# Performance work log

Hardware: AMD Instinct MI355X
Metric: run time of the kernel (lower is better)

## Reference

```python
import jax, jax.numpy as jnp
import numpy as np

N, E, IN_FT, OUT_FT = 8192, 4096, 512, 512
DENSITY = 0.02


def setup_inputs() -> dict:
    key = jax.random.key(0)
    k1, k2, k3, k4 = jax.random.split(key, 4)
    x = jax.random.normal(k1, (N, IN_FT), dtype=jnp.float32)
    hypergraph = (jax.random.uniform(k2, (N, E)) < DENSITY).astype(jnp.float32)
    # kaiming_uniform on [in, out]: fan_in = in_ft (torch fan of a Linear-style 2D param is dim 1 size? torch computes fan_in = size(1) for 2D -> out_ft here)
    bound_w = float(np.sqrt(6.0 / OUT_FT))  # kaiming_uniform a=sqrt(5)? default a=0 -> gain sqrt(2); bound = gain*sqrt(3/fan_in)
    bound_w = float(np.sqrt(2.0) * np.sqrt(3.0 / OUT_FT))
    weight = jax.random.uniform(k3, (IN_FT, OUT_FT), minval=-bound_w, maxval=bound_w, dtype=jnp.float32)
    bound_v = float(np.sqrt(2.0) * np.sqrt(3.0 / 1.0))
    V = jax.random.uniform(k4, (IN_FT, 1), minval=-bound_v, maxval=bound_v, dtype=jnp.float32)
    bias = jnp.zeros((OUT_FT,), dtype=jnp.float32)
    return {"x": x, "hypergraph": hypergraph, "weight": weight, "V": V, "bias": bias}


def reference(x, hypergraph, weight, V, bias):
    # edge embeddings: H^T @ x  -> [E, in_ft]
    edge_emb = hypergraph.T @ x
    hw = jax.nn.sigmoid(edge_emb @ V)          # [E, 1] learned hyperedge weights
    w = hw[:, 0]                                # [E]
    deg_v = (hypergraph @ hw)[:, 0]             # [N]  (sum over last dim of H @ hw)
    deg_e = jnp.sum(hypergraph, axis=0)         # [E]
    # adj = diag(deg_v) @ H @ diag(w) @ diag(deg_e) @ H^T @ diag(deg_v)
    # fused as broadcasted row/col scalings around two GEMMs (same math, no NxN)
    out = x @ weight                            # [N, out_ft]
    t = hypergraph.T @ (deg_v[:, None] * out)   # [E, out_ft]
    t = (w * deg_e)[:, None] * t                # diagonal edge scalings
    out = deg_v[:, None] * (hypergraph @ t)     # [N, out_ft]
    out = out + bias
    return (out, w)
```

## Files before the change

kernel.cpp:

```cpp
#include <hip/hip_runtime.h>


#define N_NODES 8192
#define N_EDGES 4096
#define FT 512

typedef short bf16x8 __attribute__((ext_vector_type(8)));
typedef float f32x4 __attribute__((ext_vector_type(4)));
typedef unsigned short u16;
typedef unsigned int u32;
typedef unsigned char u8;

__device__ __forceinline__ u16 f2b(float f) {
    union { float f; u32 u; } v; v.f = f;
    u32 r = v.u + 0x7FFFu + ((v.u >> 16) & 1u);
    return (u16)(r >> 16);
}
__device__ __forceinline__ float b2f(u16 h) {
    union { u32 u; float f; } v; v.u = ((u32)h) << 16; return v.f;
}
__device__ __forceinline__ u32 pack2(u32 w) {
    union { float f; u32 u; } a, b;
    a.f = (float)(w & 0xFFu);
    b.f = (float)((w >> 8) & 0xFFu);
    return __builtin_amdgcn_perm(b.u, a.u, 0x07060302u);
}


__global__ __launch_bounds__(256) void zero_kernel(float* p, int n) {
    int i = blockIdx.x * 256 + threadIdx.x;
    if (i < n) p[i] = 0.f;
}

__global__ __launch_bounds__(256) void xv_kernel(const float* __restrict__ x,
                                                 const float* __restrict__ V,
                                                 float* __restrict__ xv) {
    int row = blockIdx.x * 4 + (threadIdx.x >> 6);
    int lane = threadIdx.x & 63;
    const float* xr = x + (size_t)row * FT + lane * 8;
    const float* vr = V + lane * 8;
    float4 a0 = *(const float4*)xr, a1 = *(const float4*)(xr + 4);
    float4 b0 = *(const float4*)vr, b1 = *(const float4*)(vr + 4);
    float acc = a0.x * b0.x + a0.y * b0.y + a0.z * b0.z + a0.w * b0.w +
                a1.x * b1.x + a1.y * b1.y + a1.z * b1.z + a1.w * b1.w;
#pragma unroll
    for (int off = 32; off; off >>= 1) acc += __shfl_down(acc, off);
    if (lane == 0) xv[row] = acc;
}

__global__ __launch_bounds__(256) void cvt_colsum_kernel(const float* __restrict__ H,
                                                         const float* __restrict__ xv,
                                                         u8* __restrict__ Hu8,
                                                         float* __restrict__ zsum,
                                                         float* __restrict__ desum) {
    int e0 = (blockIdx.x * 256 + threadIdx.x) * 4;
    int n0 = blockIdx.y * 32;
    float z0 = 0.f, z1 = 0.f, z2 = 0.f, z3 = 0.f;
    float d0 = 0.f, d1 = 0.f, d2 = 0.f, d3 = 0.f;
#pragma unroll 4
    for (int i = 0; i < 32; i++) {
        int n = n0 + i;
        float4 h = *(const float4*)(H + (size_t)n * N_EDGES + e0);
        float xvn = xv[n];
        z0 += h.x * xvn; z1 += h.y * xvn; z2 += h.z * xvn; z3 += h.w * xvn;
        d0 += h.x; d1 += h.y; d2 += h.z; d3 += h.w;
        u32 p = (u32)h.x | ((u32)h.y << 8) | ((u32)h.z << 16) | ((u32)h.w << 24);
        *(u32*)(Hu8 + (size_t)n * N_EDGES + e0) = p;
    }
    atomicAdd(zsum + e0 + 0, z0); atomicAdd(zsum + e0 + 1, z1);
    atomicAdd(zsum + e0 + 2, z2); atomicAdd(zsum + e0 + 3, z3);
    atomicAdd(desum + e0 + 0, d0); atomicAdd(desum + e0 + 1, d1);
    atomicAdd(desum + e0 + 2, d2); atomicAdd(desum + e0 + 3, d3);
}

__global__ __launch_bounds__(256) void sigmoid_kernel(const float* __restrict__ zsum,
                                                      const float* __restrict__ desum,
                                                      float* __restrict__ w_out,
                                                      float* __restrict__ wde) {
    int e = blockIdx.x * 256 + threadIdx.x;
    float z = zsum[e];
    float wv = 1.f / (1.f + expf(-z));
    w_out[e] = wv;
    wde[e] = wv * desum[e];
}

__global__ __launch_bounds__(256) void degv_kernel(const u8* __restrict__ Hu8,
                                                   const float* __restrict__ w,
                                                   float* __restrict__ degv) {
    int row = blockIdx.x * 4 + (threadIdx.x >> 6);
    int lane = threadIdx.x & 63;
    const u32* hr = (const u32*)(Hu8 + (size_t)row * N_EDGES);
    const float4* wr = (const float4*)w;
    float acc = 0.f;
#pragma unroll
    for (int i = 0; i < 16; i++) {
        int idx = i * 64 + lane;
        u32 h4 = hr[idx];
        float4 ww = wr[idx];
        if (h4 & 0x000000FFu) acc += ww.x;
        if (h4 & 0x0000FF00u) acc += ww.y;
        if (h4 & 0x00FF0000u) acc += ww.z;
        if (h4 & 0xFF000000u) acc += ww.w;
    }
#pragma unroll
    for (int off = 32; off; off >>= 1) acc += __shfl_down(acc, off);
    if (lane == 0) degv[row] = acc;
}

__global__ void wt_kernel(const float* __restrict__ src, u16* __restrict__ dst) {
    __shared__ float tile[32][33];
    int tx = threadIdx.x, ty = threadIdx.y;
    int c = blockIdx.x * 32 + tx;
    int r0 = blockIdx.y * 32;
#pragma unroll
    for (int i = 0; i < 4; i++)
        tile[ty + i * 8][tx] = src[(size_t)(r0 + ty + i * 8) * FT + c];
    __syncthreads();
#pragma unroll
    for (int i = 0; i < 4; i++)
        dst[(size_t)(blockIdx.x * 32 + ty + i * 8) * FT + r0 + tx] = f2b(tile[tx][ty + i * 8]);
}

__global__ __launch_bounds__(256) void transH_kernel(const u8* __restrict__ Hu8,
                                                     u8* __restrict__ HTu8) {
    __shared__ u32 tile[64][17];
    const int t = threadIdx.x;
    const int e0 = blockIdx.x * 64, n0 = blockIdx.y * 64;
    {
        int nl = t >> 2, seg = t & 3;
        uint4 v = *(const uint4*)(Hu8 + (size_t)(n0 + nl) * N_EDGES + e0 + seg * 16);
        tile[nl][seg * 4 + 0] = v.x; tile[nl][seg * 4 + 1] = v.y;
        tile[nl][seg * 4 + 2] = v.z; tile[nl][seg * 4 + 3] = v.w;
    }
    __syncthreads();
    int ew = t >> 4, ng = t & 15;
    u32 a0 = tile[ng * 4 + 0][ew], a1 = tile[ng * 4 + 1][ew];
    u32 a2 = tile[ng * 4 + 2][ew], a3 = tile[ng * 4 + 3][ew];
#pragma unroll
    for (int i = 0; i < 4; i++) {
        u32 o = ((a0 >> (8 * i)) & 0xFFu) | (((a1 >> (8 * i)) & 0xFFu) << 8) |
                (((a2 >> (8 * i)) & 0xFFu) << 16) | (((a3 >> (8 * i)) & 0xFFu) << 24);
        *(u32*)(HTu8 + (size_t)(e0 + ew * 4 + i) * N_NODES + n0 + ng * 4) = o;
    }
}

__global__ void t2t_kernel(const u16* __restrict__ P, const float* __restrict__ wde,
                           u16* __restrict__ t2T) {
    __shared__ float tile[32][33];
    int tx = threadIdx.x, ty = threadIdx.y;
    int f0 = blockIdx.x * 32, e0 = blockIdx.y * 32;
#pragma unroll
    for (int i = 0; i < 4; i++) {
        int e = e0 + ty + i * 8;
        size_t idx = (size_t)e * 512 + f0 + tx;
        float s = 0.f;
#pragma unroll
        for (int sl = 0; sl < 8; sl++)
            s += b2f(P[idx + (size_t)sl * N_EDGES * 512]);
        tile[ty + i * 8][tx] = wde[e] * s;
    }
    __syncthreads();
#pragma unroll
    for (int i = 0; i < 4; i++)
        t2T[(size_t)(f0 + ty + i * 8) * N_EDGES + e0 + tx] = f2b(tile[tx][ty + i * 8]);
}

__global__ __launch_bounds__(256) void final_kernel(const u16* __restrict__ P,
                                                    const float* __restrict__ degv,
                                                    const float* __restrict__ bias,
                                                    float* __restrict__ out) {
    int i8 = blockIdx.x * 256 + threadIdx.x;
    int base = i8 * 8;
    int n = base >> 9, f = base & 511;
    float s[8] = {0.f, 0.f, 0.f, 0.f, 0.f, 0.f, 0.f, 0.f};
#pragma unroll
    for (int sl = 0; sl < 4; sl++) {
        uint4 v = *(const uint4*)(P + (size_t)sl * N_NODES * 512 + base);
        u32 ws[4] = {v.x, v.y, v.z, v.w};
#pragma unroll
        for (int j = 0; j < 4; j++) {
            s[2 * j]     += b2f((u16)(ws[j] & 0xFFFFu));
            s[2 * j + 1] += b2f((u16)(ws[j] >> 16));
        }
    }
    float dv = degv[n];
    float4 o0, o1;
    o0.x = dv * s[0] + bias[f + 0]; o0.y = dv * s[1] + bias[f + 1];
    o0.z = dv * s[2] + bias[f + 2]; o0.w = dv * s[3] + bias[f + 3];
    o1.x = dv * s[4] + bias[f + 4]; o1.y = dv * s[5] + bias[f + 5];
    o1.z = dv * s[6] + bias[f + 6]; o1.w = dv * s[7] + bias[f + 7];
    *(float4*)(out + base) = o0;
    *(float4*)(out + base + 4) = o1;
}


#define TBK 32

template <int MT, int NT, int ASRC, int BSRC, int EPI>
__global__ __launch_bounds__(256, 2)
void gemm5(const void* __restrict__ Ap, const void* __restrict__ Bp,
           void* __restrict__ Cp, const float* __restrict__ degv,
           int KC, int lda, int ldb, int ldc, int Msz) {
    __shared__ __align__(16) u16 Alds[MT * 32 * TBK];
    __shared__ __align__(16) u16 Blds[NT * 32 * TBK];
    const int t = threadIdx.x;
    const int m0 = blockIdx.x * (MT * 32), n0 = blockIdx.y * (NT * 32);
    const int kbase = blockIdx.z * KC;
    const int wave = t >> 6, lane = t & 63, quad = lane >> 4, lo = lane & 15;
    const int wm = (wave >> 1) * (MT * 16), wn = (wave & 1) * (NT * 16);

    f32x4 acc[MT][NT];
#pragma unroll
    for (int a = 0; a < MT; a++)
#pragma unroll
        for (int b = 0; b < NT; b++) acc[a][b] = (f32x4){0.f, 0.f, 0.f, 0.f};

    for (int kk = 0; kk < KC; kk += TBK) {
        const int k0 = kbase + kk;
        __syncthreads();
        if (ASRC == 0) {
            const u16* A = (const u16*)Ap;
#pragma unroll
            for (int i = 0; i < MT / 2; i++) {
                int c = t + i * 256;
                const u16* g = A + (size_t)(m0 + (c >> 2)) * lda + k0 + (c & 3) * 8;
                __builtin_amdgcn_global_load_lds((const u32*)g, (u32*)(Alds + c * 8), 16, 0, 0);
            }
        } else {
            const u8* A = (const u8*)Ap;
            const int r = t >> 1, h = (t & 1) * 16;
            uint4 v = *(const uint4*)(A + (size_t)(m0 + r) * lda + k0 + h);
            u32 o[8];
            o[0] = pack2(v.x); o[1] = pack2(v.x >> 16);
            o[2] = pack2(v.y); o[3] = pack2(v.y >> 16);
            o[4] = pack2(v.z); o[5] = pack2(v.z >> 16);
            o[6] = pack2(v.w); o[7] = pack2(v.w >> 16);
            *(uint4*)&Alds[r * TBK + h]     = *(uint4*)&o[0];
            *(uint4*)&Alds[r * TBK + h + 8] = *(uint4*)&o[4];
        }
        if (BSRC == 0) {
            const u16* B = (const u16*)Bp;
#pragma unroll
            for (int i = 0; i < NT / 2; i++) {
                int c = t + i * 256;
                const u16* g = B + (size_t)(n0 + (c >> 2)) * ldb + k0 + (c & 3) * 8;
                __builtin_amdgcn_global_load_lds((const u32*)g, (u32*)(Blds + c * 8), 16, 0, 0);
            }
        } else {
            const float* B = (const float*)Bp;
            const int n = t >> 1, c0 = (t & 1) * 16;
            const float4* src = (const float4*)(B + (size_t)(n0 + n) * ldb + k0 + c0);
            float4 f[4];
#pragma unroll
            for (int i = 0; i < 4; i++) f[i] = src[i];
            u16 tmp[16];
#pragma unroll
            for (int i = 0; i < 4; i++) {
                tmp[4 * i + 0] = f2b(f[i].x); tmp[4 * i + 1] = f2b(f[i].y);
                tmp[4 * i + 2] = f2b(f[i].z); tmp[4 * i + 3] = f2b(f[i].w);
            }
            *(uint4*)&Blds[n * TBK + c0]     = *(uint4*)&tmp[0];
            *(uint4*)&Blds[n * TBK + c0 + 8] = *(uint4*)&tmp[8];
        }
        __syncthreads();

        bf16x8 af[MT], bfr[NT];
#pragma unroll
        for (int mt = 0; mt < MT; mt++)
            af[mt] = *(const bf16x8*)&Alds[(wm + mt * 16 + lo) * TBK + quad * 8];
#pragma unroll
        for (int nt = 0; nt < NT; nt++)
            bfr[nt] = *(const bf16x8*)&Blds[(wn + nt * 16 + lo) * TBK + quad * 8];
#pragma unroll
        for (int mt = 0; mt < MT; mt++)
#pragma unroll
            for (int nt = 0; nt < NT; nt++)
                acc[mt][nt] = __builtin_amdgcn_mfma_f32_16x16x32_bf16(af[mt], bfr[nt], acc[mt][nt], 0, 0, 0);
    }

    if (EPI == 0) {
        u16* C = (u16*)Cp + (size_t)blockIdx.z * Msz * 512;
#pragma unroll
        for (int mt = 0; mt < MT; mt++) {
            int rb = m0 + wm + mt * 16 + quad * 4;
#pragma unroll
            for (int i = 0; i < 4; i++)
#pragma unroll
                for (int nt = 0; nt < NT; nt++)
                    C[(size_t)(rb + i) * 512 + n0 + wn + nt * 16 + lo] = f2b(acc[mt][nt][i]);
        }
    } else {
        u16* C = (u16*)Cp;
        float dv[NT];
#pragma unroll
        for (int nt = 0; nt < NT; nt++) dv[nt] = degv[n0 + wn + nt * 16 + lo];
#pragma unroll
        for (int mt = 0; mt < MT; mt++) {
            int rb = m0 + wm + mt * 16 + quad * 4;
#pragma unroll
            for (int i = 0; i < 4; i++)
#pragma unroll
                for (int nt = 0; nt < NT; nt++)
                    C[(size_t)(rb + i) * ldc + n0 + wn + nt * 16 + lo] =
                        f2b(acc[mt][nt][i] * dv[nt]);
        }
    }
}


extern "C" void kernel_launch(void* const* d_in, const int* in_sizes, int n_in,
                              void* d_out, int out_size, void* d_ws, size_t ws_size,
                              hipStream_t stream) {
    const float* x    = (const float*)d_in[0];
    const float* H    = (const float*)d_in[1];
    const float* W    = (const float*)d_in[2];
    const float* V    = (const float*)d_in[3];
    const float* bias = (const float*)d_in[4];
    float* out  = (float*)d_out;
    float* wout = out + (size_t)N_NODES * FT;
    (void)in_sizes; (void)n_in; (void)out_size; (void)ws_size;

    char* wsb = (char*)d_ws;
    float* wsf   = (float*)d_ws;
    float* xv    = wsf;
    float* zsum  = wsf + 8192;
    float* desum = wsf + 12288;
    float* wde   = wsf + 16384;
    float* degv  = wsf + 20480;
    u8*    Hu8   = (u8*)(wsb + 114688);
    u8*    HTu8  = (u8*)(wsb + 33669120);
    u16*   WT    = (u16*)(wsb + 67223552);
    u16*   doutT = (u16*)(wsb + 67747840);
    u16*   t2T   = (u16*)(wsb + 76136448);
    u16*   P     = (u16*)(wsb + 80330752);

    zero_kernel<<<32, 256, 0, stream>>>(zsum, 8192);
    xv_kernel<<<N_NODES / 4, 256, 0, stream>>>(x, V, xv);
    cvt_colsum_kernel<<<dim3(4, 256), 256, 0, stream>>>(H, xv, Hu8, zsum, desum);
    sigmoid_kernel<<<N_EDGES / 256, 256, 0, stream>>>(zsum, desum, wout, wde);
    degv_kernel<<<N_NODES / 4, 256, 0, stream>>>(Hu8, wout, degv);
    wt_kernel<<<dim3(16, 16), dim3(32, 8), 0, stream>>>(W, WT);
    transH_kernel<<<dim3(N_EDGES / 64, N_NODES / 64), 256, 0, stream>>>(Hu8, HTu8);

    gemm5<2, 4, 0, 2, 1><<<dim3(FT / 64, N_NODES / 128, 1), 256, 0, stream>>>(
        WT, x, doutT, degv, FT, FT, FT, N_NODES, 0);

    gemm5<4, 8, 1, 0, 0><<<dim3(N_EDGES / 128, FT / 256, 8), 256, 0, stream>>>(
        HTu8, doutT, P, nullptr, N_NODES / 8, N_NODES, N_NODES, 512, N_EDGES);

    t2t_kernel<<<dim3(FT / 32, N_EDGES / 32), dim3(32, 8), 0, stream>>>(P, wde, t2T);

    gemm5<4, 8, 1, 0, 0><<<dim3(N_NODES / 128, FT / 256, 4), 256, 0, stream>>>(
        Hu8, t2T, P, nullptr, N_EDGES / 4, N_EDGES, N_EDGES, 512, N_NODES);

    final_kernel<<<(N_NODES * FT / 8) / 256, 256, 0, stream>>>(P, degv, bias, out);
}
```

Baseline: 386.8 us.

## Store incidence and x as bf16 so GEMMs use direct global-to-LDS loads

The incidence matrix and its transpose are now stored as bf16 instead of u8, and x is pre-converted to bf16 inside the xv kernel. All GEMM operand loads can therefore use global_load_lds directly, with no in-register unpacking or fp32 conversion. The GEMM tiles also change from 4x8 to 4x4 with more N blocks, and the occupancy hint goes from 2 to 3. This doubles the memory traffic and footprint for H and H^T and adds an extra bf16 copy of x, in exchange for removing conversion work from the GEMM inner loops.

```diff
diff --git a/kernel.cpp b/kernel.cpp
--- a/kernel.cpp
+++ b/kernel.cpp
@@ -9,7 +9,6 @@
 typedef float f32x4 __attribute__((ext_vector_type(4)));
 typedef unsigned short u16;
 typedef unsigned int u32;
-typedef unsigned char u8;
 
 __device__ __forceinline__ u16 f2b(float f) {
     union { float f; u32 u; } v; v.f = f;
@@ -19,12 +18,6 @@
 __device__ __forceinline__ float b2f(u16 h) {
     union { u32 u; float f; } v; v.u = ((u32)h) << 16; return v.f;
 }
-__device__ __forceinline__ u32 pack2(u32 w) {
-    union { float f; u32 u; } a, b;
-    a.f = (float)(w & 0xFFu);
-    b.f = (float)((w >> 8) & 0xFFu);
-    return __builtin_amdgcn_perm(b.u, a.u, 0x07060302u);
-}
 
 
 __global__ __launch_bounds__(256) void zero_kernel(float* p, int n) {
@@ -32,9 +25,10 @@
     if (i < n) p[i] = 0.f;
 }
 
-__global__ __launch_bounds__(256) void xv_kernel(const float* __restrict__ x,
-                                                 const float* __restrict__ V,
-                                                 float* __restrict__ xv) {
+__global__ __launch_bounds__(256) void xv_xb_kernel(const float* __restrict__ x,
+                                                    const float* __restrict__ V,
+                                                    float* __restrict__ xv,
+                                                    u16* __restrict__ xb) {
     int row = blockIdx.x * 4 + (threadIdx.x >> 6);
     int lane = threadIdx.x & 63;
     const float* xr = x + (size_t)row * FT + lane * 8;
@@ -43,6 +37,9 @@
     float4 b0 = *(const float4*)vr, b1 = *(const float4*)(vr + 4);
     float acc = a0.x * b0.x + a0.y * b0.y + a0.z * b0.z + a0.w * b0.w +
                 a1.x * b1.x + a1.y * b1.y + a1.z * b1.z + a1.w * b1.w;
+    u16 tmp[8] = {f2b(a0.x), f2b(a0.y), f2b(a0.z), f2b(a0.w),
+                  f2b(a1.x), f2b(a1.y), f2b(a1.z), f2b(a1.w)};
+    *(uint4*)(xb + (size_t)row * FT + lane * 8) = *(uint4*)tmp;
 #pragma unroll
     for (int off = 32; off; off >>= 1) acc += __shfl_down(acc, off);
     if (lane == 0) xv[row] = acc;
@@ -50,7 +47,7 @@
 
 __global__ __launch_bounds__(256) void cvt_colsum_kernel(const float* __restrict__ H,
                                                          const float* __restrict__ xv,
-                                                         u8* __restrict__ Hu8,
+                                                         u16* __restrict__ Hbf,
                                                          float* __restrict__ zsum,
                                                          float* __restrict__ desum) {
     int e0 = (blockIdx.x * 256 + threadIdx.x) * 4;
@@ -64,8 +61,10 @@
         float xvn = xv[n];
         z0 += h.x * xvn; z1 += h.y * xvn; z2 += h.z * xvn; z3 += h.w * xvn;
         d0 += h.x; d1 += h.y; d2 += h.z; d3 += h.w;
-        u32 p = (u32)h.x | ((u32)h.y << 8) | ((u32)h.z << 16) | ((u32)h.w << 24);
-        *(u32*)(Hu8 + (size_t)n * N_EDGES + e0) = p;
+        uint2 p;
+        p.x = (h.x != 0.f ? 0x3F80u : 0u) | (h.y != 0.f ? 0x3F800000u : 0u);
+        p.y = (h.z != 0.f ? 0x3F80u : 0u) | (h.w != 0.f ? 0x3F800000u : 0u);
+        *(uint2*)(Hbf + (size_t)n * N_EDGES + e0) = p;
     }
     atomicAdd(zsum + e0 + 0, z0); atomicAdd(zsum + e0 + 1, z1);
     atomicAdd(zsum + e0 + 2, z2); atomicAdd(zsum + e0 + 3, z3);
@@ -84,23 +83,23 @@
     wde[e] = wv * desum[e];
 }
 
-__global__ __launch_bounds__(256) void degv_kernel(const u8* __restrict__ Hu8,
+__global__ __launch_bounds__(256) void degv_kernel(const u16* __restrict__ Hbf,
                                                    const float* __restrict__ w,
                                                    float* __restrict__ degv) {
     int row = blockIdx.x * 4 + (threadIdx.x >> 6);
     int lane = threadIdx.x & 63;
-    const u32* hr = (const u32*)(Hu8 + (size_t)row * N_EDGES);
-    const float4* wr = (const float4*)w;
+    const uint4* hr = (const uint4*)(Hbf + (size_t)row * N_EDGES);
     float acc = 0.f;
 #pragma unroll
-    for (int i = 0; i < 16; i++) {
+    for (int i = 0; i < 8; i++) {
         int idx = i * 64 + lane;
-        u32 h4 = hr[idx];
-        float4 ww = wr[idx];
-        if (h4 & 0x000000FFu) acc += ww.x;
-        if (h4 & 0x0000FF00u) acc += ww.y;
-        if (h4 & 0x00FF0000u) acc += ww.z;
-        if (h4 & 0xFF000000u) acc += ww.w;
+        uint4 h = hr[idx];
+        const float* w8 = w + idx * 8;
+        float4 wa = *(const float4*)w8, wb = *(const float4*)(w8 + 4);
+        if (h.x & 0xFFFFu) acc += wa.x;  if (h.x >> 16) acc += wa.y;
+        if (h.y & 0xFFFFu) acc += wa.z;  if (h.y >> 16) acc += wa.w;
+        if (h.z & 0xFFFFu) acc += wb.x;  if (h.z >> 16) acc += wb.y;
+        if (h.w & 0xFFFFu) acc += wb.z;  if (h.w >> 16) acc += wb.w;
     }
 #pragma unroll
     for (int off = 32; off; off >>= 1) acc += __shfl_down(acc, off);
@@ -121,26 +120,36 @@
         dst[(size_t)(blockIdx.x * 32 + ty + i * 8) * FT + r0 + tx] = f2b(tile[tx][ty + i * 8]);
 }
 
-__global__ __launch_bounds__(256) void transH_kernel(const u8* __restrict__ Hu8,
-                                                     u8* __restrict__ HTu8) {
-    __shared__ u32 tile[64][17];
+__global__ __launch_bounds__(256) void transHb_kernel(const u16* __restrict__ Hbf,
+                                                      u16* __restrict__ HTbf) {
+    __shared__ u32 Wt[64][33];
     const int t = threadIdx.x;
     const int e0 = blockIdx.x * 64, n0 = blockIdx.y * 64;
     {
-        int nl = t >> 2, seg = t & 3;
-        uint4 v = *(const uint4*)(Hu8 + (size_t)(n0 + nl) * N_EDGES + e0 + seg * 16);
-        tile[nl][seg * 4 + 0] = v.x; tile[nl][seg * 4 + 1] = v.y;
-        tile[nl][seg * 4 + 2] = v.z; tile[nl][seg * 4 + 3] = v.w;
+        int n = t >> 2, seg = t & 3;
+        const u16* src = Hbf + (size_t)(n0 + n) * N_EDGES + e0;
+#pragma unroll
+        for (int jj = 0; jj < 2; jj++) {
+            int j = seg + jj * 4;
+            uint4 v = *(const uint4*)(src + j * 8);
+            Wt[n][j * 4 + 0] = v.x; Wt[n][j * 4 + 1] = v.y;
+            Wt[n][j * 4 + 2] = v.z; Wt[n][j * 4 + 3] = v.w;
+        }
     }
     __syncthreads();
-    int ew = t >> 4, ng = t & 15;
-    u32 a0 = tile[ng * 4 + 0][ew], a1 = tile[ng * 4 + 1][ew];
-    u32 a2 = tile[ng * 4 + 2][ew], a3 = tile[ng * 4 + 3][ew];
-#pragma unroll
-    for (int i = 0; i < 4; i++) {
-        u32 o = ((a0 >> (8 * i)) & 0xFFu) | (((a1 >> (8 * i)) & 0xFFu) << 8) |
-                (((a2 >> (8 * i)) & 0xFFu) << 16) | (((a3 >> (8 * i)) & 0xFFu) << 24);
-        *(u32*)(HTu8 + (size_t)(e0 + ew * 4 + i) * N_NODES + n0 + ng * 4) = o;
+    {
+        int e = t >> 2, g = t & 3;
+        int ew = e >> 1;
+        u32 sel = (e & 1) ? 0x07060302u : 0x05040100u;
+        u32* drow = (u32*)(HTbf + (size_t)(e0 + e) * N_NODES + n0);
+        u32 o[8];
+#pragma unroll
+        for (int j = 0; j < 8; j++) {
+            int np = g * 8 + j;
+            o[j] = __builtin_amdgcn_perm(Wt[2 * np + 1][ew], Wt[2 * np][ew], sel);
+        }
+        *(uint4*)(drow + g * 8)     = *(uint4*)&o[0];
+        *(uint4*)(drow + g * 8 + 4) = *(uint4*)&o[4];
     }
 }
 
@@ -196,9 +205,9 @@
 
 #define TBK 32
 
-template <int MT, int NT, int ASRC, int BSRC, int EPI>
-__global__ __launch_bounds__(256, 2)
-void gemm5(const void* __restrict__ Ap, const void* __restrict__ Bp,
+template <int MT, int NT, int EPI>
+__global__ __launch_bounds__(256, 3)
+void gemm6(const u16* __restrict__ Ap, const u16* __restrict__ Bp,
            void* __restrict__ Cp, const float* __restrict__ degv,
            int KC, int lda, int ldb, int ldc, int Msz) {
     __shared__ __align__(16) u16 Alds[MT * 32 * TBK];
@@ -218,49 +227,17 @@
     for (int kk = 0; kk < KC; kk += TBK) {
         const int k0 = kbase + kk;
         __syncthreads();
-        if (ASRC == 0) {
-            const u16* A = (const u16*)Ap;
-#pragma unroll
-            for (int i = 0; i < MT / 2; i++) {
-                int c = t + i * 256;
-                const u16* g = A + (size_t)(m0 + (c >> 2)) * lda + k0 + (c & 3) * 8;
-                __builtin_amdgcn_global_load_lds((const u32*)g, (u32*)(Alds + c * 8), 16, 0, 0);
-            }
-        } else {
-            const u8* A = (const u8*)Ap;
-            const int r = t >> 1, h = (t & 1) * 16;
-            uint4 v = *(const uint4*)(A + (size_t)(m0 + r) * lda + k0 + h);
-            u32 o[8];
-            o[0] = pack2(v.x); o[1] = pack2(v.x >> 16);
-            o[2] = pack2(v.y); o[3] = pack2(v.y >> 16);
-            o[4] = pack2(v.z); o[5] = pack2(v.z >> 16);
-            o[6] = pack2(v.w); o[7] = pack2(v.w >> 16);
-            *(uint4*)&Alds[r * TBK + h]     = *(uint4*)&o[0];
-            *(uint4*)&Alds[r * TBK + h + 8] = *(uint4*)&o[4];
-        }
-        if (BSRC == 0) {
-            const u16* B = (const u16*)Bp;
-#pragma unroll
-            for (int i = 0; i < NT / 2; i++) {
-                int c = t + i * 256;
-                const u16* g = B + (size_t)(n0 + (c >> 2)) * ldb + k0 + (c & 3) * 8;
-                __builtin_amdgcn_global_load_lds((const u32*)g, (u32*)(Blds + c * 8), 16, 0, 0);
-            }
-        } else {
-            const float* B = (const float*)Bp;
-            const int n = t >> 1, c0 = (t & 1) * 16;
-            const float4* src = (const float4*)(B + (size_t)(n0 + n) * ldb + k0 + c0);
-            float4 f[4];
-#pragma unroll
-            for (int i = 0; i < 4; i++) f[i] = src[i];
-            u16 tmp[16];
-#pragma unroll
-            for (int i = 0; i < 4; i++) {
-                tmp[4 * i + 0] = f2b(f[i].x); tmp[4 * i + 1] = f2b(f[i].y);
-                tmp[4 * i + 2] = f2b(f[i].z); tmp[4 * i + 3] = f2b(f[i].w);
-            }
-            *(uint4*)&Blds[n * TBK + c0]     = *(uint4*)&tmp[0];
-            *(uint4*)&Blds[n * TBK + c0 + 8] = *(uint4*)&tmp[8];
+#pragma unroll
+        for (int i = 0; i < MT / 2; i++) {
+            int c = t + i * 256;
+            const u16* g = Ap + (size_t)(m0 + (c >> 2)) * lda + k0 + (c & 3) * 8;
+            __builtin_amdgcn_global_load_lds((const u32*)g, (u32*)(Alds + c * 8), 16, 0, 0);
+        }
+#pragma unroll
+        for (int i = 0; i < NT / 2; i++) {
+            int c = t + i * 256;
+            const u16* g = Bp + (size_t)(n0 + (c >> 2)) * ldb + k0 + (c & 3) * 8;
+            __builtin_amdgcn_global_load_lds((const u32*)g, (u32*)(Blds + c * 8), 16, 0, 0);
         }
         __syncthreads();
 
@@ -327,31 +304,32 @@
     float* desum = wsf + 12288;
     float* wde   = wsf + 16384;
     float* degv  = wsf + 20480;
-    u8*    Hu8   = (u8*)(wsb + 114688);
-    u8*    HTu8  = (u8*)(wsb + 33669120);
-    u16*   WT    = (u16*)(wsb + 67223552);
-    u16*   doutT = (u16*)(wsb + 67747840);
-    u16*   t2T   = (u16*)(wsb + 76136448);
-    u16*   P     = (u16*)(wsb + 80330752);
+    u16*   Hbf   = (u16*)(wsb + 114688);
+    u16*   HTbf  = (u16*)(wsb + 67223552);
+    u16*   WT    = (u16*)(wsb + 134332416);
+    u16*   doutT = (u16*)(wsb + 134856704);
+    u16*   t2T   = (u16*)(wsb + 143245312);
+    u16*   xb    = (u16*)(wsb + 147439616);
+    u16*   P     = (u16*)(wsb + 155828224);
 
     zero_kernel<<<32, 256, 0, stream>>>(zsum, 8192);
-    xv_kernel<<<N_NODES / 4, 256, 0, stream>>>(x, V, xv);
-    cvt_colsum_kernel<<<dim3(4, 256), 256, 0, stream>>>(H, xv, Hu8, zsum, desum);
+    xv_xb_kernel<<<N_NODES / 4, 256, 0, stream>>>(x, V, xv, xb);
+    cvt_colsum_kernel<<<dim3(4, 256), 256, 0, stream>>>(H, xv, Hbf, zsum, desum);
     sigmoid_kernel<<<N_EDGES / 256, 256, 0, stream>>>(zsum, desum, wout, wde);
-    degv_kernel<<<N_NODES / 4, 256, 0, stream>>>(Hu8, wout, degv);
+    degv_kernel<<<N_NODES / 4, 256, 0, stream>>>(Hbf, wout, degv);
     wt_kernel<<<dim3(16, 16), dim3(32, 8), 0, stream>>>(W, WT);
-    transH_kernel<<<dim3(N_EDGES / 64, N_NODES / 64), 256, 0, stream>>>(Hu8, HTu8);
-
-    gemm5<2, 4, 0, 2, 1><<<dim3(FT / 64, N_NODES / 128, 1), 256, 0, stream>>>(
-        WT, x, doutT, degv, FT, FT, FT, N_NODES, 0);
-
-    gemm5<4, 8, 1, 0, 0><<<dim3(N_EDGES / 128, FT / 256, 8), 256, 0, stream>>>(
-        HTu8, doutT, P, nullptr, N_NODES / 8, N_NODES, N_NODES, 512, N_EDGES);
+    transHb_kernel<<<dim3(N_EDGES / 64, N_NODES / 64), 256, 0, stream>>>(Hbf, HTbf);
+
+    gemm6<2, 4, 1><<<dim3(FT / 64, N_NODES / 128, 1), 256, 0, stream>>>(
+        WT, xb, doutT, degv, FT, FT, FT, N_NODES, 0);
+
+    gemm6<4, 4, 0><<<dim3(N_EDGES / 128, FT / 128, 8), 256, 0, stream>>>(
+        HTbf, doutT, P, nullptr, N_NODES / 8, N_NODES, N_NODES, 512, N_EDGES);
 
     t2t_kernel<<<dim3(FT / 32, N_EDGES / 32), dim3(32, 8), 0, stream>>>(P, wde, t2T);
 
-    gemm5<4, 8, 1, 0, 0><<<dim3(N_NODES / 128, FT / 256, 4), 256, 0, stream>>>(
-        Hu8, t2T, P, nullptr, N_EDGES / 4, N_EDGES, N_EDGES, 512, N_NODES);
+    gemm6<4, 4, 0><<<dim3(N_NODES / 128, FT / 128, 4), 256, 0, stream>>>(
+        Hbf, t2T, P, nullptr, N_EDGES / 4, N_EDGES, N_EDGES, 512, N_NODES);
 
     final_kernel<<<(N_NODES * FT / 8) / 256, 256, 0, stream>>>(P, degv, bias, out);
 }
```

Result: no change. 391.3 us (+1.2%).
